# Kernel optimization log

Hardware: AMD Instinct MI355X
Metric: run time of the kernel (lower is better)

Reference implementation:

```python
import jax, jax.numpy as jnp
import numpy as np

B = 16        # graphs per batch
N0 = 4096     # nodes per graph (equal-size graphs -> static TopK shapes)
DEG = 8       # avg degree
E = B * N0 * DEG
CW = 64
OUT = 256


def _seg_sum(vals, idx, n):
    return jax.ops.segment_sum(vals, idx, num_segments=n)


def _sage(x, src, dst, valid, wl, bl, wr, n):
    # PyG SAGEConv: lin_l(mean_{j->i} x_j) + lin_r(x_i); lin_r has no bias
    vf = valid.astype(x.dtype)
    msg = x[src] * vf[:, None]                     # [E, d]
    s = _seg_sum(msg, dst, n)
    cnt = _seg_sum(vf, dst, n)
    mean = s / jnp.maximum(cnt, 1.0)[:, None]
    return mean @ wl.T + bl + x @ wr.T


def _gcn(x, src, dst, valid, w, b, n):
    # PyG GCNConv: add self-loops, symmetric normalization
    h = x @ w.T
    vf = valid.astype(x.dtype)
    deg = 1.0 + _seg_sum(vf, dst, n)               # includes self-loop
    inv_sqrt = jax.lax.rsqrt(deg)
    norm = inv_sqrt[src] * inv_sqrt[dst] * vf      # [E]
    agg = _seg_sum(h[src] * norm[:, None], dst, n) + h * (1.0 / deg)[:, None]
    return agg + b


def _topk_pool(x, src, dst, valid, w, n_per_graph):
    # PyG TopKPooling: score = x@w/||w||, keep top ceil(ratio*n) per graph,
    # x' = x[perm] * tanh(score[perm]); reindex edges, drop edges with removed endpoints.
    k = (n_per_graph + 1) // 2
    score = (x @ w) / jnp.linalg.norm(w)
    vals, idx = jax.lax.top_k(score.reshape(B, n_per_graph), k)   # [B,k]
    offs = (jnp.arange(B, dtype=jnp.int32) * n_per_graph)[:, None]
    perm = (idx.astype(jnp.int32) + offs).reshape(-1)             # [B*k] global ids
    x_new = x[perm] * jnp.tanh(vals.reshape(-1))[:, None]
    new_idx = jnp.full((B * n_per_graph,), -1, dtype=jnp.int32).at[perm].set(
        jnp.arange(B * k, dtype=jnp.int32))
    s2, d2 = new_idx[src], new_idx[dst]
    valid2 = valid & (s2 >= 0) & (d2 >= 0)
    s2 = jnp.where(valid2, s2, 0)
    d2 = jnp.where(valid2, d2, 0)
    return x_new, s2, d2, valid2, k


def _readout(x, k):
    xg = x.reshape(B, k, -1)
    return jnp.concatenate([xg.max(axis=1), xg.mean(axis=1)], axis=1)  # [B, 2d]


def _forward(x, edge_src, edge_dst, w1_l, b1, w1_r, w2_l, b2, w2_r, w3_l, b3, w3_r,
             w4, b4, w5, b5, w6, b6, p1, p2, p3, p4, p5, p6,
             lw1, lb1, lw2, lb2, lw3, lb3):
    src, dst = edge_src, edge_dst
    valid = jnp.ones((E,), dtype=bool)
    n = N0
    sage_ps = [(w1_l, b1, w1_r), (w2_l, b2, w2_r), (w3_l, b3, w3_r)]
    gcn_ps = [(w4, b4), (w5, b5), (w6, b6)]
    pools = [p1, p2, p3, p4, p5, p6]
    h = x
    z = None
    for i in range(6):
        if i < 3:
            wl, bl, wr = sage_ps[i]
            h = jax.nn.relu(_sage(h, src, dst, valid, wl, bl, wr, B * n))
        else:
            w, b = gcn_ps[i - 3]
            h = jax.nn.relu(_gcn(h, src, dst, valid, w, b, B * n))
        h, src, dst, valid, n = _topk_pool(h, src, dst, valid, pools[i], n)
        r = _readout(h, n)
        z = r if z is None else z + r
    z = jax.nn.relu(z @ lw1.T + lb1)
    z = jax.nn.relu(z @ lw2.T + lb2)
    z = z @ lw3.T + lb3
    return jax.nn.softmax(z, axis=1)


def setup_inputs() -> dict:
    key = jax.random.key(0)
    ks = jax.random.split(key, 40)

    def nrm(k, shape, s=0.1):
        return jax.random.normal(k, shape, dtype=jnp.float32) * s

    # per-graph random edges (both endpoints inside the same graph block)
    epg = N0 * DEG
    src_l = jax.random.randint(ks[0], (B, epg), 0, N0, dtype=jnp.int32)
    dst_l = jax.random.randint(ks[1], (B, epg), 0, N0, dtype=jnp.int32)
    offs = (jnp.arange(B, dtype=jnp.int32) * N0)[:, None]
    inp = {
        'x': jax.random.normal(ks[2], (B * N0, 2), dtype=jnp.float32),
        'edge_src': (src_l + offs).reshape(-1),
        'edge_dst': (dst_l + offs).reshape(-1),
        'w1_l': nrm(ks[3], (CW, 2)), 'b1': nrm(ks[4], (CW,)), 'w1_r': nrm(ks[5], (CW, 2)),
        'w2_l': nrm(ks[6], (CW, CW)), 'b2': nrm(ks[7], (CW,)), 'w2_r': nrm(ks[8], (CW, CW)),
        'w3_l': nrm(ks[9], (CW, CW)), 'b3': nrm(ks[10], (CW,)), 'w3_r': nrm(ks[11], (CW, CW)),
        'w4': nrm(ks[12], (CW, CW)), 'b4': jnp.zeros((CW,), jnp.float32),
        'w5': nrm(ks[13], (CW, CW)), 'b5': jnp.zeros((CW,), jnp.float32),
        'w6': nrm(ks[14], (CW, CW)), 'b6': jnp.zeros((CW,), jnp.float32),
        'p1': nrm(ks[15], (CW,)), 'p2': nrm(ks[16], (CW,)), 'p3': nrm(ks[17], (CW,)),
        'p4': nrm(ks[18], (CW,)), 'p5': nrm(ks[19], (CW,)), 'p6': nrm(ks[20], (CW,)),
        'lw1': nrm(ks[21], (128, 2 * CW)), 'lb1': nrm(ks[22], (128,)),
        'lw2': nrm(ks[23], (64, 128)), 'lb2': nrm(ks[24], (64,)),
        'lw3': nrm(ks[25], (OUT, 64)), 'lb3': nrm(ks[26], (OUT,)),
    }
    return inp


def reference(x, edge_src, edge_dst, w1_l, b1, w1_r, w2_l, b2, w2_r, w3_l, b3, w3_r,
              w4, b4, w5, b5, w6, b6, p1, p2, p3, p4, p5, p6,
              lw1, lb1, lw2, lb2, lw3, lb3):
    return _forward(x, edge_src, edge_dst, w1_l, b1, w1_r, w2_l, b2, w2_r,
                    w3_l, b3, w3_r, w4, b4, w5, b5, w6, b6,
                    p1, p2, p3, p4, p5, p6, lw1, lb1, lw2, lb2, lw3, lb3)
```

## Files before the change

### kernel.cpp

```cpp
#include <hip/hip_runtime.h>
#include <math.h>

#define NB 16
#define N0 4096
#define NE 524288
#define CAPE 1280


static __global__ void k_count(const int* __restrict__ dst, int* __restrict__ cnt) {
  int e = blockIdx.x * 256 + threadIdx.x;
  if (e >= NE) return;
  atomicAdd(&cnt[dst[e]], 1);
}

static __global__ void k_fill0(const int* __restrict__ src, const int* __restrict__ dst,
                               int* __restrict__ cursor, int* __restrict__ list) {
  int e = blockIdx.x * 256 + threadIdx.x;
  if (e >= NE) return;
  int d = dst[e];
  int slot = atomicAdd(&cursor[d], 1);
  list[slot] = src[e];
}


static __global__ void k_scan1(const int* __restrict__ in, int* __restrict__ out,
                               int* __restrict__ bsum, int n) {
  __shared__ int ts[256];
  int base = blockIdx.x * 1024 + threadIdx.x * 4;
  int a0 = (base + 0 < n) ? in[base + 0] : 0;
  int a1 = (base + 1 < n) ? in[base + 1] : 0;
  int a2 = (base + 2 < n) ? in[base + 2] : 0;
  int a3 = (base + 3 < n) ? in[base + 3] : 0;
  int s = a0 + a1 + a2 + a3;
  ts[threadIdx.x] = s;
  __syncthreads();
  for (int off = 1; off < 256; off <<= 1) {
    int v = (threadIdx.x >= off) ? ts[threadIdx.x - off] : 0;
    __syncthreads();
    ts[threadIdx.x] += v;
    __syncthreads();
  }
  int excl = ts[threadIdx.x] - s;
  if (base + 0 < n) out[base + 0] = excl;
  excl += a0;
  if (base + 1 < n) out[base + 1] = excl;
  excl += a1;
  if (base + 2 < n) out[base + 2] = excl;
  excl += a2;
  if (base + 3 < n) out[base + 3] = excl;
  if (threadIdx.x == 255) bsum[blockIdx.x] = ts[255];
}

static __global__ void k_scan3(int* __restrict__ out, int* __restrict__ out2,
                               const int* __restrict__ bsum, int n, int nblk) {
  __shared__ int sb[64];
  int t = threadIdx.x;
  if (t < 64) {
    int v = (t < nblk) ? bsum[t] : 0;
    int p = v;
    for (int off = 1; off < 64; off <<= 1) {
      int u = __shfl_up(p, off);
      if (t >= off) p += u;
    }
    sb[t] = p - v;
  }
  __syncthreads();
  int i = blockIdx.x * 256 + t;
  if (i < n) {
    int v = out[i] + sb[i >> 10];
    out[i] = v;
    if (out2) out2[i] = v;
  }
}


static __global__ void k_newfill(const int* __restrict__ perm, const int* __restrict__ offs,
                                 const int* __restrict__ cnt, const int* __restrict__ list,
                                 const int* __restrict__ newidx, const int* __restrict__ noffs,
                                 int* __restrict__ nlist, int newn) {
  int nn = blockIdx.x * 256 + threadIdx.x;
  if (nn >= newn) return;
  int old = perm[nn];
  int st = offs[old], c = cnt[old];
  int pos = noffs[nn];
  for (int j = 0; j < c; ++j) {
    int s2 = newidx[list[st + j]];
    if (s2 >= 0) nlist[pos++] = s2;
  }
}


static __global__ void k_pw(const float* __restrict__ p0, const float* __restrict__ p1,
                            const float* __restrict__ p2, const float* __restrict__ p3,
                            const float* __restrict__ p4, const float* __restrict__ p5,
                            const float* __restrict__ w0, const float* __restrict__ w1,
                            const float* __restrict__ w2, const float* __restrict__ w3,
                            const float* __restrict__ w4, const float* __restrict__ w5,
                            const float* __restrict__ w6, float* __restrict__ pnbuf,
                            float* __restrict__ wp) {
  if (blockIdx.x < 6) {
    if (threadIdx.x >= 64) return;
    const float* pp = p0;
    switch (blockIdx.x) {
      case 1: pp = p1; break;
      case 2: pp = p2; break;
      case 3: pp = p3; break;
      case 4: pp = p4; break;
      case 5: pp = p5; break;
      default: break;
    }
    double v = (double)pp[threadIdx.x];
    v *= v;
#pragma unroll
    for (int off = 1; off < 64; off <<= 1) v += __shfl_xor(v, off);
    if (threadIdx.x == 0) pnbuf[blockIdx.x] = (float)(1.0 / sqrt(v));
  } else {
    int wi = blockIdx.x - 6;
    const float* src = w0;
    switch (wi) {
      case 1: src = w1; break;
      case 2: src = w2; break;
      case 3: src = w3; break;
      case 4: src = w4; break;
      case 5: src = w5; break;
      case 6: src = w6; break;
      default: break;
    }
    float* dst = wp + (size_t)wi * 4096;
    const float4* w4p = (const float4*)src;
    for (int i4 = threadIdx.x; i4 < 1024; i4 += 256) {
      int o = i4 >> 4, db = (i4 & 15) << 2;
      float4 W = w4p[i4];
      float Wv[4] = {W.x, W.y, W.z, W.w};
      int og = o >> 2, o3 = o & 3;
#pragma unroll
      for (int j = 0; j < 4; ++j) {
        int d = db + j;
        dst[(d << 6) + (((og ^ (d & 15)) << 2) | o3)] = Wv[j];
      }
    }
  }
}


static __global__ void k_sage_gather2(const float* __restrict__ x, const int* __restrict__ offs,
                                      const int* __restrict__ cnt, const int* __restrict__ list,
                                      float* __restrict__ mean, int ntot) {
  int v = blockIdx.x * 256 + threadIdx.x;
  if (v >= ntot) return;
  int st = offs[v], c = cnt[v];
  float s0 = 0.f, s1 = 0.f;
  for (int j = 0; j < c; ++j) {
    int s = list[st + j];
    s0 += x[s * 2 + 0];
    s1 += x[s * 2 + 1];
  }
  float inv = 1.0f / fmaxf((float)c, 1.0f);
  mean[v * 2 + 0] = s0 * inv;
  mean[v * 2 + 1] = s1 * inv;
}

static __global__ void k_sage0(const float* __restrict__ x, const float* __restrict__ mean,
                               const float* __restrict__ wl, const float* __restrict__ blv,
                               const float* __restrict__ wr, const float* __restrict__ pvec,
                               const float* __restrict__ pnbuf, float* __restrict__ h,
                               float* __restrict__ score, int ntot) {
  __shared__ float wlT[2][65], wrT[2][65];
  if (threadIdx.x < 128) {
    int o = threadIdx.x >> 1, d = threadIdx.x & 1;
    wlT[d][o] = wl[o * 2 + d];
    wrT[d][o] = wr[o * 2 + d];
  }
  __syncthreads();
  int o = threadIdx.x & 63, vl = threadIdx.x >> 6;
  int base = blockIdx.x * 16 + vl * 4;
  float pn = pnbuf[0];
  float psl = pvec[o];
#pragma unroll
  for (int r = 0; r < 4; ++r) {
    int v = base + r;
    if (v >= ntot) break;
    float acc = blv[o] + mean[v * 2 + 0] * wlT[0][o] + mean[v * 2 + 1] * wlT[1][o] +
                x[v * 2 + 0] * wrT[0][o] + x[v * 2 + 1] * wrT[1][o];
    float hval = fmaxf(acc, 0.0f);
    h[(size_t)v * 64 + o] = hval;
    double sc = (double)hval * (double)psl;
#pragma unroll
    for (int off = 1; off < 64; off <<= 1) sc += __shfl_xor(sc, off);
    if (o == 0) score[v] = (float)sc * pn;
  }
}

static __global__ __launch_bounds__(512) void k_sage_mm(
    const float* __restrict__ x, const int* __restrict__ offs, const int* __restrict__ cnt,
    const int* __restrict__ list, const float* __restrict__ wlT, const float* __restrict__ blv,
    const float* __restrict__ wrT, const float* __restrict__ pvec,
    const float* __restrict__ pnbuf, int pidx, float* __restrict__ h,
    float* __restrict__ score) {
  __shared__ float smem[8192];
  __shared__ float psh[64], bsh[64];
  __shared__ int lds_list[CAPE];
  float* xT = smem;
  float* mT = smem + 4096;
  int t = threadIdx.x;
  size_t nb = (size_t)((blockIdx.x & 7) * (gridDim.x >> 3) + (blockIdx.x >> 3));

  if (t < 64) {
    psh[t] = pvec[t];
    bsh[t] = blv[t];
  }
  const float4* x4 = (const float4*)(x + nb * 4096);
  for (int i = t; i < 1024; i += 512) {
    int node = i >> 4, db = (i & 15) << 2;
    float4 a = x4[i];
    float av[4] = {a.x, a.y, a.z, a.w};
    int ng = node >> 2, n0 = node & 3;
#pragma unroll
    for (int j = 0; j < 4; ++j) {
      int d = db + j;
      xT[(d << 6) + (((ng ^ (d & 15)) << 2) | n0)] = av[j];
    }
  }
  int gv0 = (int)nb * 64;
  int st0 = offs[gv0];
  int nedge = offs[gv0 + 63] + cnt[gv0 + 63] - st0;
  int ncap = (nedge < CAPE) ? nedge : CAPE;
  for (int e = t; e < ncap; e += 512) lds_list[e] = list[st0 + e];
  __syncthreads();

  {
    int lane = t & 63, w = t >> 6;
    int stq[8], cq[8];
    float accq[8];
    int cmax = 0;
#pragma unroll
    for (int q = 0; q < 8; ++q) {
      int gv = gv0 + w * 8 + q;
      stq[q] = offs[gv] - st0;
      cq[q] = cnt[gv];
      accq[q] = 0.f;
      cmax = max(cmax, cq[q]);
    }
    int ncl = (nedge > 0) ? (nedge - 1) : 0;
    for (int j = 0; j < cmax; ++j) {
#pragma unroll
      for (int q = 0; q < 8; ++q) {
        bool act = j < cq[q];
        int idx = stq[q] + (act ? j : 0);
        idx = (idx < ncl) ? idx : ncl;
        int sn = (idx < ncap) ? lds_list[idx] : list[st0 + idx];
        float xv = x[(size_t)(sn & 32767) * 64 + lane];
        accq[q] = act ? (accq[q] + xv) : accq[q];
      }
    }
#pragma unroll
    for (int q = 0; q < 8; ++q) {
      int node = w * 8 + q;
      float mval = accq[q] * (1.0f / fmaxf((float)cq[q], 1.0f));
      int col = (((node >> 2) ^ (lane & 15)) << 2) | (node & 3);
      mT[(lane << 6) + col] = mval;
    }
  }
  __syncthreads();

  int tx = t & 15, ty = t >> 4;
  int ng = ty >> 1, n0 = (ty & 1) << 1;
  float acc[2][4] = {};
#pragma unroll 4
  for (int k = 0; k < 64; ++k) {
    int s = k & 15;
    int ca = (((ng ^ s) << 2) | n0);
    const float2 a2 = *(const float2*)&xT[(k << 6) + ca];
    const float2 m2 = *(const float2*)&mT[(k << 6) + ca];
    const float4 L = *(const float4*)&wlT[(k << 6) + ((tx ^ s) << 2)];
    const float4 R = *(const float4*)&wrT[(k << 6) + ((tx ^ s) << 2)];
    float A[2] = {a2.x, a2.y}, M[2] = {m2.x, m2.y};
    float Lv[4] = {L.x, L.y, L.z, L.w}, Rv[4] = {R.x, R.y, R.z, R.w};
#pragma unroll
    for (int r = 0; r < 2; ++r)
#pragma unroll
      for (int c = 0; c < 4; ++c) acc[r][c] += M[r] * Lv[c] + A[r] * Rv[c];
  }

  float pn = pnbuf[pidx];
  float hv[2][4];
  double sp[2];
#pragma unroll
  for (int r = 0; r < 2; ++r) {
    sp[r] = 0.0;
#pragma unroll
    for (int c = 0; c < 4; ++c) {
      float v = fmaxf(acc[r][c] + bsh[(tx << 2) + c], 0.0f);
      hv[r][c] = v;
      sp[r] += (double)v * (double)psh[(tx << 2) + c];
    }
  }
  __syncthreads();
  float* hT = smem;
  double* sred = (double*)(smem + 4608);
#pragma unroll
  for (int r = 0; r < 2; ++r) {
    int node = (ty << 1) + r;
    int nk = node & 15;
#pragma unroll
    for (int c = 0; c < 4; ++c) hT[node * 68 + (((tx ^ nk) << 2) | c)] = hv[r][c];
    sred[(tx << 6) + node] = sp[r];
  }
  __syncthreads();
  float4* h4 = (float4*)(h + nb * 4096);
  for (int i = t; i < 1024; i += 512) {
    int node = i >> 4, q = i & 15;
    h4[i] = *(const float4*)&hT[node * 68 + ((q ^ (node & 15)) << 2)];
  }
  if (t < 64) {
    double ssum = 0.0;
    for (int g = 0; g < 16; ++g) ssum += sred[(g << 6) + t];
    score[nb * 64 + t] = (float)ssum * pn;
  }
}


static __global__ __launch_bounds__(256) void k_gcn_mm(const float* __restrict__ x,
                                                       const float* __restrict__ wT,
                                                       float* __restrict__ h1) {
  __shared__ float smem[4608];
  float* xT = smem;
  int t = threadIdx.x;
  size_t nb = blockIdx.x;
  const float4* x4 = (const float4*)(x + nb * 4096);
  for (int i = t; i < 1024; i += 256) {
    int node = i >> 4, db = (i & 15) << 2;
    float4 a = x4[i];
    float av[4] = {a.x, a.y, a.z, a.w};
    int ng = node >> 2, n0 = node & 3;
#pragma unroll
    for (int j = 0; j < 4; ++j) {
      int d = db + j;
      xT[(d << 6) + (((ng ^ (d & 15)) << 2) | n0)] = av[j];
    }
  }
  __syncthreads();
  int tx = t & 15, ty = t >> 4;
  float acc[4][4] = {};
#pragma unroll 4
  for (int k = 0; k < 64; ++k) {
    int s = k & 15;
    const float4 a = *(const float4*)&xT[(k << 6) + ((tx ^ s) << 2)];
    const float4 W = *(const float4*)&wT[(k << 6) + ((ty ^ s) << 2)];
    float A[4] = {a.x, a.y, a.z, a.w}, Wv[4] = {W.x, W.y, W.z, W.w};
#pragma unroll
    for (int r = 0; r < 4; ++r)
#pragma unroll
      for (int c = 0; c < 4; ++c) acc[r][c] += A[r] * Wv[c];
  }
  __syncthreads();
  float* hT = smem;
#pragma unroll
  for (int r = 0; r < 4; ++r) {
    int node = (tx << 2) + r;
    int nk = node & 15;
#pragma unroll
    for (int c = 0; c < 4; ++c) hT[node * 68 + (((ty ^ nk) << 2) | c)] = acc[r][c];
  }
  __syncthreads();
  float4* h4 = (float4*)(h1 + nb * 4096);
  for (int i = t; i < 1024; i += 256) {
    int node = i >> 4, q = i & 15;
    h4[i] = *(const float4*)&hT[node * 68 + ((q ^ (node & 15)) << 2)];
  }
}

static __global__ void k_gcn_gather(const float* __restrict__ h1, const int* __restrict__ offs,
                                    const int* __restrict__ cnt, const int* __restrict__ list,
                                    const float* __restrict__ b, const float* __restrict__ pvec,
                                    const float* __restrict__ pnbuf, int pidx,
                                    float* __restrict__ h, float* __restrict__ score, int ntot) {
  int lane = threadIdx.x & 63, vl = threadIdx.x >> 6;
  int v = blockIdx.x * 4 + vl;
  if (v >= ntot) return;
  int st = offs[v], c = cnt[v];
  float degv = 1.0f + (float)c;
  float ivd = 1.0f / sqrtf(degv);
  float acc = 0.f;
  for (int j = 0; j < c; ++j) {
    int s = list[st + j];
    float nrm = (1.0f / sqrtf(1.0f + (float)cnt[s])) * ivd;
    acc += h1[(size_t)s * 64 + lane] * nrm;
  }
  float outv = fmaxf(acc + h1[(size_t)v * 64 + lane] * (1.0f / degv) + b[lane], 0.0f);
  h[(size_t)v * 64 + lane] = outv;
  double sc = (double)outv * (double)pvec[lane];
#pragma unroll
  for (int off = 1; off < 64; off <<= 1) sc += __shfl_xor(sc, off);
  if (lane == 0) score[v] = (float)sc * pnbuf[pidx];
}


static __global__ void k_chunksort(const float* __restrict__ score,
                                   unsigned long long* __restrict__ runs, int n_per, int k,
                                   int* __restrict__ newidx, int* __restrict__ perm, int single) {
  extern __shared__ unsigned long long sk[];
  int CH = blockDim.x;
  int g0 = blockIdx.x * CH;
  int b = g0 / n_per;
  int i = threadIdx.x;
  int gi = g0 + i;
  int li = gi - b * n_per;
  unsigned u = __float_as_uint(score[gi]);
  unsigned s = (u & 0x80000000u) ? u : ~(u | 0x80000000u);
  sk[i] = ((unsigned long long)s << 32) | (unsigned)li;
  __syncthreads();
  for (int ksz = 2; ksz <= CH; ksz <<= 1) {
    for (int j = ksz >> 1; j > 0; j >>= 1) {
      int ixj = i ^ j;
      if (ixj > i) {
        unsigned long long a = sk[i], c = sk[ixj];
        bool up = ((i & ksz) == 0);
        if ((a > c) == up) {
          sk[i] = c;
          sk[ixj] = a;
        }
      }
      __syncthreads();
    }
  }
  if (!single) {
    runs[gi] = sk[i];
  } else {
    int r = i;
    int idx = (int)(sk[r] & 0xFFFFFFFFu);
    int gidx = b * n_per + idx;
    if (r < k) {
      perm[b * k + r] = gidx;
      newidx[gidx] = b * k + r;
    } else {
      newidx[gidx] = -1;
    }
  }
}

static __global__ void k_merge(const unsigned long long* __restrict__ in,
                               unsigned long long* __restrict__ out, int L, int ntot, int n_per,
                               int k, int* __restrict__ newidx, int* __restrict__ perm,
                               int final) {
  int g = blockIdx.x * 256 + threadIdx.x;
  if (g >= ntot) return;
  unsigned long long key = in[g];
  int pair = g / (2 * L);
  int base = pair * 2 * L;
  int t = g - base;
  const unsigned long long* sib;
  int p;
  if (t < L) {
    sib = in + base + L;
    p = t;
  } else {
    sib = in + base;
    p = t - L;
  }
  int lo = 0, hi = L;
  while (lo < hi) {
    int mid = (lo + hi) >> 1;
    lo = (sib[mid] < key) ? mid + 1 : lo;
    hi = (sib[mid] < key) ? hi : mid;
  }
  int pos = p + lo;
  if (!final) {
    out[base + pos] = key;
  } else {
    int b = base / n_per;
    int idx = (int)(key & 0xFFFFFFFFu);
    int gidx = b * n_per + idx;
    if (pos < k) {
      perm[b * k + pos] = gidx;
      newidx[gidx] = b * k + pos;
    } else {
      newidx[gidx] = -1;
    }
  }
}


static __global__ __launch_bounds__(1024) void k_pool_post(
    const float* __restrict__ h, const float* __restrict__ score, const int* __restrict__ perm,
    float* __restrict__ xnew, float* __restrict__ pmax, float* __restrict__ psum, int base,
    const int* __restrict__ offs, const int* __restrict__ cnt, const int* __restrict__ list,
    const int* __restrict__ newidx, int* __restrict__ ncnt, int newn, int G1) {
  __shared__ float tile[64 * 68];
  __shared__ float pm[16][65], ps[16][65];
  int t = threadIdx.x;
  if ((int)blockIdx.x >= G1) {
    int nn = ((int)blockIdx.x - G1) * 1024 + t;
    if (nn >= newn) return;
    int old = perm[nn];
    int st = offs[old], c = cnt[old];
    int cc = 0;
    for (int j = 0; j < c; ++j) cc += (newidx[list[st + j]] >= 0);
    ncnt[nn] = cc;
    return;
  }
  int node = t >> 4, q = t & 15;
  int nn = blockIdx.x * 64 + node;
  int old = perm[nn];
  float tm = tanhf(score[old]);
  float4 v = *(const float4*)&h[(size_t)old * 64 + q * 4];
  v.x *= tm;
  v.y *= tm;
  v.z *= tm;
  v.w *= tm;
  *(float4*)&xnew[(size_t)nn * 64 + q * 4] = v;
  *(float4*)&tile[node * 68 + ((q ^ (node & 15)) << 2)] = v;
  __syncthreads();
  int slot = t >> 6, d = t & 63;
  int q2 = d >> 2, i3 = d & 3;
  float m = -INFINITY, s = 0.f;
#pragma unroll
  for (int r = 0; r < 4; ++r) {
    int nd = slot * 4 + r;
    float val = tile[nd * 68 + (((q2 ^ (nd & 15)) << 2) | i3)];
    m = fmaxf(m, val);
    s += val;
  }
  pm[slot][d] = m;
  ps[slot][d] = s;
  __syncthreads();
  if (t < 64) {
    float mm = -INFINITY, ss = 0.f;
#pragma unroll
    for (int sl = 0; sl < 16; ++sl) {
      mm = fmaxf(mm, pm[sl][t]);
      ss += ps[sl][t];
    }
    pmax[(size_t)(base + blockIdx.x) * 64 + t] = mm;
    psum[(size_t)(base + blockIdx.x) * 64 + t] = ss;
  }
}


static __global__ void k_mlp(const float* __restrict__ pmax, const float* __restrict__ psum,
                             const float* __restrict__ lw1, const float* __restrict__ lb1,
                             const float* __restrict__ lw2, const float* __restrict__ lb2,
                             const float* __restrict__ lw3, const float* __restrict__ lb3,
                             float* __restrict__ out) {
  __shared__ float zs[128], t1[128], t2[64], t3[256], red[256];
  int b = blockIdx.x, tid = threadIdx.x;
  const int baseL[6] = {0, 512, 768, 896, 960, 992};
  const int nchL[6] = {32, 16, 8, 4, 2, 1};
  const int kkL[6] = {2048, 1024, 512, 256, 128, 64};
  if (tid < 64) {
    float zm = 0.f;
    for (int i = 0; i < 6; ++i) {
      float m = -INFINITY;
      for (int c = 0; c < nchL[i]; ++c)
        m = fmaxf(m, pmax[(size_t)(baseL[i] + b * nchL[i] + c) * 64 + tid]);
      zm += m;
    }
    zs[tid] = zm;
  } else if (tid < 128) {
    int d = tid - 64;
    float zsum = 0.f;
    for (int i = 0; i < 6; ++i) {
      float s = 0.f;
      for (int c = 0; c < nchL[i]; ++c)
        s += psum[(size_t)(baseL[i] + b * nchL[i] + c) * 64 + d];
      zsum += s / (float)kkL[i];
    }
    zs[tid] = zsum;
  }
  __syncthreads();
  if (tid < 128) {
    double a = 0.0;
    for (int d = 0; d < 128; ++d) a += (double)lw1[tid * 128 + d] * (double)zs[d];
    t1[tid] = fmaxf((float)a + lb1[tid], 0.0f);
  }
  __syncthreads();
  if (tid < 64) {
    double a = 0.0;
    for (int d = 0; d < 128; ++d) a += (double)lw2[tid * 128 + d] * (double)t1[d];
    t2[tid] = fmaxf((float)a + lb2[tid], 0.0f);
  }
  __syncthreads();
  {
    double a = 0.0;
    for (int d = 0; d < 64; ++d) a += (double)lw3[tid * 64 + d] * (double)t2[d];
    t3[tid] = (float)a + lb3[tid];
  }
  __syncthreads();
  red[tid] = t3[tid];
  __syncthreads();
  for (int s = 128; s > 0; s >>= 1) {
    if (tid < s) red[tid] = fmaxf(red[tid], red[tid + s]);
    __syncthreads();
  }
  float mx = red[0];
  __syncthreads();
  float e = expf(t3[tid] - mx);
  red[tid] = e;
  __syncthreads();
  for (int s = 128; s > 0; s >>= 1) {
    if (tid < s) red[tid] += red[tid + s];
    __syncthreads();
  }
  out[b * 256 + tid] = e / red[0];
}


extern "C" void kernel_launch(void* const* d_in, const int* in_sizes, int n_in,
                              void* d_out, int out_size, void* d_ws, size_t ws_size,
                              hipStream_t stream) {
  const float* x0 = (const float*)d_in[0];
  const int* esrc0 = (const int*)d_in[1];
  const int* edst0 = (const int*)d_in[2];
  const float* WL[3] = {(const float*)d_in[3], (const float*)d_in[6], (const float*)d_in[9]};
  const float* BL[3] = {(const float*)d_in[4], (const float*)d_in[7], (const float*)d_in[10]};
  const float* WR[3] = {(const float*)d_in[5], (const float*)d_in[8], (const float*)d_in[11]};
  const float* WG[3] = {(const float*)d_in[12], (const float*)d_in[14], (const float*)d_in[16]};
  const float* BG[3] = {(const float*)d_in[13], (const float*)d_in[15], (const float*)d_in[17]};
  const float* P[6] = {(const float*)d_in[18], (const float*)d_in[19], (const float*)d_in[20],
                       (const float*)d_in[21], (const float*)d_in[22], (const float*)d_in[23]};
  const float* lw1 = (const float*)d_in[24];
  const float* lb1 = (const float*)d_in[25];
  const float* lw2 = (const float*)d_in[26];
  const float* lb2 = (const float*)d_in[27];
  const float* lw3 = (const float*)d_in[28];
  const float* lb3 = (const float*)d_in[29];

  char* ws = (char*)d_ws;
  size_t off = 0;
  auto alloc = [&](size_t bytes) -> void* {
    void* p = ws + off;
    off += (bytes + 255) & ~(size_t)255;
    return p;
  };
  float* hA = (float*)alloc((size_t)65536 * 64 * 4);
  float* hB = (float*)alloc((size_t)32768 * 64 * 4);
  float* mean = (float*)alloc((size_t)65536 * 2 * 4);
  float* tmp = (float*)alloc((size_t)8192 * 64 * 4);
  float* score = (float*)alloc((size_t)65536 * 4);
  int* newidx = (int*)alloc((size_t)65536 * 4);
  int* perm = (int*)alloc((size_t)32768 * 4);
  int* cntA = (int*)alloc((size_t)65536 * 4);
  int* cntB = (int*)alloc((size_t)65536 * 4);
  int* offsA = (int*)alloc((size_t)65536 * 4);
  int* offsB = (int*)alloc((size_t)65536 * 4);
  int* cursor = (int*)alloc((size_t)65536 * 4);
  int* bsum = (int*)alloc((size_t)64 * 4);
  int* listA = (int*)alloc((size_t)NE * 4);
  int* listB = (int*)alloc((size_t)NE * 4);
  float* pmax = (float*)alloc((size_t)1024 * 64 * 4);
  float* psum = (float*)alloc((size_t)1024 * 64 * 4);
  unsigned long long* keyA = (unsigned long long*)alloc((size_t)65536 * 8);
  unsigned long long* keyB = (unsigned long long*)alloc((size_t)65536 * 8);
  float* pnbuf = (float*)alloc((size_t)64 * 4);
  float* wp = (float*)alloc((size_t)7 * 4096 * 4);
  if (off > ws_size) return;

  auto scan = [&](int* cntp, int* offsp, int* curp, int n) {
    int nblk = (n + 1023) / 1024;
    k_scan1<<<nblk, 256, 0, stream>>>(cntp, offsp, bsum, n);
    k_scan3<<<(n + 255) / 256, 256, 0, stream>>>(offsp, curp, bsum, n, nblk);
  };

  k_pw<<<13, 256, 0, stream>>>(P[0], P[1], P[2], P[3], P[4], P[5], WL[1], WR[1], WL[2], WR[2],
                               WG[0], WG[1], WG[2], pnbuf, wp);

  hipMemsetAsync(cntA, 0, (size_t)65536 * 4, stream);
  k_count<<<NE / 256, 256, 0, stream>>>(edst0, cntA);
  scan(cntA, offsA, cursor, 65536);
  k_fill0<<<NE / 256, 256, 0, stream>>>(esrc0, edst0, cursor, listA);

  const float* xcur = x0;
  int* ccnt = cntA;
  int* coffs = offsA;
  int* clist = listA;
  const int baseL[6] = {0, 512, 768, 896, 960, 992};

  for (int i = 0; i < 6; ++i) {
    int n_per = N0 >> i;
    int ntot = NB * n_per;
    int k = n_per >> 1;

    if (i == 0) {
      k_sage_gather2<<<(ntot + 255) / 256, 256, 0, stream>>>(xcur, coffs, ccnt, clist, mean, ntot);
      k_sage0<<<(ntot + 15) / 16, 256, 0, stream>>>(xcur, mean, WL[0], BL[0], WR[0], P[0], pnbuf,
                                                    hA, score, ntot);
    } else if (i < 3) {
      const float* wlp = wp + (size_t)((i - 1) * 2 + 0) * 4096;
      const float* wrp = wp + (size_t)((i - 1) * 2 + 1) * 4096;
      k_sage_mm<<<ntot / 64, 512, 0, stream>>>(xcur, coffs, ccnt, clist, wlp, BL[i], wrp, P[i],
                                               pnbuf, i, hA, score);
    } else {
      int g = i - 3;
      k_gcn_mm<<<ntot / 64, 256, 0, stream>>>(xcur, wp + (size_t)(4 + g) * 4096, tmp);
      k_gcn_gather<<<(ntot + 3) / 4, 256, 0, stream>>>(tmp, coffs, ccnt, clist, BG[g], P[i],
                                                       pnbuf, i, hA, score, ntot);
    }

    int CH = (n_per < 1024) ? n_per : 1024;
    int single = (CH == n_per) ? 1 : 0;
    k_chunksort<<<ntot / CH, CH, (size_t)CH * 8, stream>>>(score, keyA, n_per, k, newidx, perm,
                                                           single);
    if (!single) {
      unsigned long long* cur = keyA;
      unsigned long long* nxt = keyB;
      for (int L = CH; L * 2 <= n_per; L <<= 1) {
        int fin = (L * 2 == n_per) ? 1 : 0;
        k_merge<<<(ntot + 255) / 256, 256, 0, stream>>>(cur, nxt, L, ntot, n_per, k, newidx, perm,
                                                        fin);
        unsigned long long* t2 = cur;
        cur = nxt;
        nxt = t2;
      }
    }

    int nch = k / 64;
    int G1 = NB * nch;
    int newn = (i < 5) ? NB * k : 0;
    int* ncnt = (i & 1) ? cntA : cntB;
    int G2 = (newn > 0) ? (newn + 1023) / 1024 : 0;
    k_pool_post<<<G1 + G2, 1024, 0, stream>>>(hA, score, perm, hB, pmax, psum, baseL[i], coffs,
                                              ccnt, clist, newidx, ncnt, newn, G1);

    if (i < 5) {
      int* noffs = (i & 1) ? offsA : offsB;
      int* nlist = (i & 1) ? listA : listB;
      scan(ncnt, noffs, nullptr, newn);
      k_newfill<<<(newn + 255) / 256, 256, 0, stream>>>(perm, coffs, ccnt, clist, newidx, noffs,
                                                        nlist, newn);
      ccnt = ncnt;
      coffs = noffs;
      clist = nlist;
    }

    xcur = hB;
  }

  k_mlp<<<NB, 256, 0, stream>>>(pmax, psum, lw1, lb1, lw2, lb2, lw3, lb3, (float*)d_out);
}
```

Baseline: 351.6 us.

## Fuse SAGE mean gather into layer-0 kernel and use sentinel edge lists for deep levels

The separate mean-gather kernel for the first SAGE layer is removed. Two lanes of each 64-lane node group now compute the neighbour mean inline and broadcast it by shuffle, which drops a launch and the intermediate mean buffer. For pooling levels 2–4, the scan plus compaction fill is replaced by remapping every edge-list entry through newidx inside the pool_post launch. Removed neighbours become -1 sentinels, and separate offset and length arrays are kept. This cuts several small launches per level, but the later gathers walk uncompacted lists with sentinels, and the remap touches the full edge-array size each level.

```diff
diff --git a/kernel.cpp b/kernel.cpp
--- a/kernel.cpp
+++ b/kernel.cpp
@@ -143,24 +143,8 @@
 }
 
 
-static __global__ void k_sage_gather2(const float* __restrict__ x, const int* __restrict__ offs,
-                                      const int* __restrict__ cnt, const int* __restrict__ list,
-                                      float* __restrict__ mean, int ntot) {
-  int v = blockIdx.x * 256 + threadIdx.x;
-  if (v >= ntot) return;
-  int st = offs[v], c = cnt[v];
-  float s0 = 0.f, s1 = 0.f;
-  for (int j = 0; j < c; ++j) {
-    int s = list[st + j];
-    s0 += x[s * 2 + 0];
-    s1 += x[s * 2 + 1];
-  }
-  float inv = 1.0f / fmaxf((float)c, 1.0f);
-  mean[v * 2 + 0] = s0 * inv;
-  mean[v * 2 + 1] = s1 * inv;
-}
-
-static __global__ void k_sage0(const float* __restrict__ x, const float* __restrict__ mean,
+static __global__ void k_sage0(const float* __restrict__ x, const int* __restrict__ offs,
+                               const int* __restrict__ cnt, const int* __restrict__ list,
                                const float* __restrict__ wl, const float* __restrict__ blv,
                                const float* __restrict__ wr, const float* __restrict__ pvec,
                                const float* __restrict__ pnbuf, float* __restrict__ h,
@@ -180,8 +164,21 @@
   for (int r = 0; r < 4; ++r) {
     int v = base + r;
     if (v >= ntot) break;
-    float acc = blv[o] + mean[v * 2 + 0] * wlT[0][o] + mean[v * 2 + 1] * wlT[1][o] +
-                x[v * 2 + 0] * wrT[0][o] + x[v * 2 + 1] * wrT[1][o];
+    float mv = 0.f;
+    {
+      int st = offs[v], c = cnt[v];
+      if (o < 2) {
+        float s = 0.f;
+        for (int j = 0; j < c; ++j) {
+          int sn = list[st + j];
+          s += x[sn * 2 + o];
+        }
+        mv = s * (1.0f / fmaxf((float)c, 1.0f));
+      }
+    }
+    float m0 = __shfl(mv, 0), m1 = __shfl(mv, 1);
+    float acc = blv[o] + m0 * wlT[0][o] + m1 * wlT[1][o] + x[v * 2 + 0] * wrT[0][o] +
+                x[v * 2 + 1] * wrT[1][o];
     float hval = fmaxf(acc, 0.0f);
     h[(size_t)v * 64 + o] = hval;
     double sc = (double)hval * (double)psl;
@@ -371,21 +368,24 @@
 }
 
 static __global__ void k_gcn_gather(const float* __restrict__ h1, const int* __restrict__ offs,
-                                    const int* __restrict__ cnt, const int* __restrict__ list,
-                                    const float* __restrict__ b, const float* __restrict__ pvec,
+                                    const int* __restrict__ lenarr, const int* __restrict__ vcnt,
+                                    const int* __restrict__ list, const float* __restrict__ b,
+                                    const float* __restrict__ pvec,
                                     const float* __restrict__ pnbuf, int pidx,
                                     float* __restrict__ h, float* __restrict__ score, int ntot) {
   int lane = threadIdx.x & 63, vl = threadIdx.x >> 6;
   int v = blockIdx.x * 4 + vl;
   if (v >= ntot) return;
-  int st = offs[v], c = cnt[v];
-  float degv = 1.0f + (float)c;
+  int st = offs[v], len = lenarr[v];
+  float degv = 1.0f + (float)vcnt[v];
   float ivd = 1.0f / sqrtf(degv);
   float acc = 0.f;
-  for (int j = 0; j < c; ++j) {
-    int s = list[st + j];
-    float nrm = (1.0f / sqrtf(1.0f + (float)cnt[s])) * ivd;
-    acc += h1[(size_t)s * 64 + lane] * nrm;
+  for (int j = 0; j < len; ++j) {
+    int e = list[st + j];
+    if (e >= 0) {
+      float nrm = (1.0f / sqrtf(1.0f + (float)vcnt[e])) * ivd;
+      acc += h1[(size_t)e * 64 + lane] * nrm;
+    }
   }
   float outv = fmaxf(acc + h1[(size_t)v * 64 + lane] * (1.0f / degv) + b[lane], 0.0f);
   h[(size_t)v * 64 + lane] = outv;
@@ -484,24 +484,44 @@
 static __global__ __launch_bounds__(1024) void k_pool_post(
     const float* __restrict__ h, const float* __restrict__ score, const int* __restrict__ perm,
     float* __restrict__ xnew, float* __restrict__ pmax, float* __restrict__ psum, int base,
-    const int* __restrict__ offs, const int* __restrict__ cnt, const int* __restrict__ list,
-    const int* __restrict__ newidx, int* __restrict__ ncnt, int newn, int G1) {
+    const int* __restrict__ offs, const int* __restrict__ lenarr, const int* __restrict__ list,
+    const int* __restrict__ newidx, int* __restrict__ ncnt, int* __restrict__ noffs,
+    int* __restrict__ nlen, int newn, int G1, int G2, const int* __restrict__ rin,
+    int* __restrict__ rout, int rn) {
   __shared__ float tile[64 * 68];
   __shared__ float pm[16][65], ps[16][65];
   int t = threadIdx.x;
-  if ((int)blockIdx.x >= G1) {
-    int nn = ((int)blockIdx.x - G1) * 1024 + t;
+  int bid = blockIdx.x;
+  if (bid >= G1 + G2) {
+    int e = (bid - G1 - G2) * 1024 + t;
+    if (e < rn) {
+      int v = rin[e];
+      rout[e] = (v >= 0 && v < 65536) ? newidx[v] : -1;
+    }
+    return;
+  }
+  if (bid >= G1) {
+    int nn = (bid - G1) * 1024 + t;
     if (nn >= newn) return;
     int old = perm[nn];
-    int st = offs[old], c = cnt[old];
+    int st = offs[old], c = lenarr[old];
     int cc = 0;
-    for (int j = 0; j < c; ++j) cc += (newidx[list[st + j]] >= 0);
+    for (int j = 0; j < c; ++j) {
+      int e = list[st + j];
+      cc += (e >= 0 && newidx[e] >= 0);
+    }
     ncnt[nn] = cc;
     return;
   }
   int node = t >> 4, q = t & 15;
-  int nn = blockIdx.x * 64 + node;
+  int nn = bid * 64 + node;
   int old = perm[nn];
+  if (noffs && t < 64) {
+    int nn2 = bid * 64 + t;
+    int o2 = perm[nn2];
+    noffs[nn2] = offs[o2];
+    nlen[nn2] = lenarr[o2];
+  }
   float tm = tanhf(score[old]);
   float4 v = *(const float4*)&h[(size_t)old * 64 + q * 4];
   v.x *= tm;
@@ -531,8 +551,8 @@
       mm = fmaxf(mm, pm[sl][t]);
       ss += ps[sl][t];
     }
-    pmax[(size_t)(base + blockIdx.x) * 64 + t] = mm;
-    psum[(size_t)(base + blockIdx.x) * 64 + t] = ss;
+    pmax[(size_t)(base + bid) * 64 + t] = mm;
+    psum[(size_t)(base + bid) * 64 + t] = ss;
   }
 }
 
@@ -634,7 +654,6 @@
   };
   float* hA = (float*)alloc((size_t)65536 * 64 * 4);
   float* hB = (float*)alloc((size_t)32768 * 64 * 4);
-  float* mean = (float*)alloc((size_t)65536 * 2 * 4);
   float* tmp = (float*)alloc((size_t)8192 * 64 * 4);
   float* score = (float*)alloc((size_t)65536 * 4);
   int* newidx = (int*)alloc((size_t)65536 * 4);
@@ -643,6 +662,8 @@
   int* cntB = (int*)alloc((size_t)65536 * 4);
   int* offsA = (int*)alloc((size_t)65536 * 4);
   int* offsB = (int*)alloc((size_t)65536 * 4);
+  int* lenA = (int*)alloc((size_t)32768 * 4);
+  int* lenB = (int*)alloc((size_t)32768 * 4);
   int* cursor = (int*)alloc((size_t)65536 * 4);
   int* bsum = (int*)alloc((size_t)64 * 4);
   int* listA = (int*)alloc((size_t)NE * 4);
@@ -673,6 +694,7 @@
   int* ccnt = cntA;
   int* coffs = offsA;
   int* clist = listA;
+  int* clen = nullptr;
   const int baseL[6] = {0, 512, 768, 896, 960, 992};
 
   for (int i = 0; i < 6; ++i) {
@@ -681,9 +703,8 @@
     int k = n_per >> 1;
 
     if (i == 0) {
-      k_sage_gather2<<<(ntot + 255) / 256, 256, 0, stream>>>(xcur, coffs, ccnt, clist, mean, ntot);
-      k_sage0<<<(ntot + 15) / 16, 256, 0, stream>>>(xcur, mean, WL[0], BL[0], WR[0], P[0], pnbuf,
-                                                    hA, score, ntot);
+      k_sage0<<<(ntot + 15) / 16, 256, 0, stream>>>(xcur, coffs, ccnt, clist, WL[0], BL[0],
+                                                    WR[0], P[0], pnbuf, hA, score, ntot);
     } else if (i < 3) {
       const float* wlp = wp + (size_t)((i - 1) * 2 + 0) * 4096;
       const float* wrp = wp + (size_t)((i - 1) * 2 + 1) * 4096;
@@ -692,8 +713,9 @@
     } else {
       int g = i - 3;
       k_gcn_mm<<<ntot / 64, 256, 0, stream>>>(xcur, wp + (size_t)(4 + g) * 4096, tmp);
-      k_gcn_gather<<<(ntot + 3) / 4, 256, 0, stream>>>(tmp, coffs, ccnt, clist, BG[g], P[i],
-                                                       pnbuf, i, hA, score, ntot);
+      k_gcn_gather<<<(ntot + 3) / 4, 256, 0, stream>>>(tmp, coffs, clen ? clen : ccnt, ccnt,
+                                                       clist, BG[g], P[i], pnbuf, i, hA, score,
+                                                       ntot);
     }
 
     int CH = (n_per < 1024) ? n_per : 1024;
@@ -716,20 +738,33 @@
     int nch = k / 64;
     int G1 = NB * nch;
     int newn = (i < 5) ? NB * k : 0;
+    int compacted_out = (i < 2);
+    int sentinel_out = (i >= 2 && i < 5);
     int* ncnt = (i & 1) ? cntA : cntB;
+    int* noffs = (i & 1) ? offsA : offsB;
+    int* nlen = (i & 1) ? lenA : lenB;
+    int* nlist = (i & 1) ? listA : listB;
     int G2 = (newn > 0) ? (newn + 1023) / 1024 : 0;
-    k_pool_post<<<G1 + G2, 1024, 0, stream>>>(hA, score, perm, hB, pmax, psum, baseL[i], coffs,
-                                              ccnt, clist, newidx, ncnt, newn, G1);
-
-    if (i < 5) {
-      int* noffs = (i & 1) ? offsA : offsB;
-      int* nlist = (i & 1) ? listA : listB;
+    int G3 = sentinel_out ? (NE / 1024) : 0;
+    const int* lenarr = clen ? clen : ccnt;
+    k_pool_post<<<G1 + G2 + G3, 1024, 0, stream>>>(
+        hA, score, perm, hB, pmax, psum, baseL[i], coffs, lenarr, clist, newidx, ncnt,
+        sentinel_out ? noffs : nullptr, sentinel_out ? nlen : nullptr, newn, G1, G2, clist,
+        nlist, G3 ? NE : 0);
+
+    if (compacted_out) {
       scan(ncnt, noffs, nullptr, newn);
       k_newfill<<<(newn + 255) / 256, 256, 0, stream>>>(perm, coffs, ccnt, clist, newidx, noffs,
                                                         nlist, newn);
       ccnt = ncnt;
       coffs = noffs;
       clist = nlist;
+      clen = nullptr;
+    } else if (sentinel_out) {
+      ccnt = ncnt;
+      coffs = noffs;
+      clist = nlist;
+      clen = nlen;
     }
 
     xcur = hB;
```

Measured after the change: 355.8 us. About the same (+1.2%).
